# Kernel tuning notes

Measured on AMD Instinct MI355X. Metric: run time of the kernel, lower is better.

## Reference

```python
import jax, jax.numpy as jnp
import numpy as np

EPS = 1e-4
HEADS = 8
DIM_HEAD = 32
BALANCE = 0.3


def _normalize(x, dims):
    # torch normalize(): norm over `dims` in fp32; norm = eps + norm*sqrt(norm.numel()/x.numel())
    red = 1
    for d in dims:
        red *= x.shape[d]
    norm = jnp.sqrt(jnp.sum(jnp.square(x.astype(jnp.float32)), axis=dims, keepdims=True))
    norm = EPS + norm / np.sqrt(red)
    return x / norm.astype(x.dtype)


def _mpconv1x1(x, w, gain=1.0):
    # MPConv forward (eval mode): weight-normalize per output channel, scale, 1x1 conv
    w = w.astype(jnp.float32)
    w = _normalize(w, (1, 2, 3))
    fan_in = w.shape[1] * w.shape[2] * w.shape[3]
    w = (w * (gain / np.sqrt(fan_in))).astype(x.dtype)[:, :, 0, 0]  # [out, in]
    return jnp.einsum('oi,nihw->nohw', w, x)


def setup_inputs() -> dict:
    key = jax.random.key(0)
    k1, k2, k3 = jax.random.split(key, 3)
    x = jax.random.normal(k1, (2, 256, 48, 48), dtype=jnp.float32)
    w_qkv = jax.random.normal(k2, (768, 256, 1, 1), dtype=jnp.float32)
    w_out = jax.random.normal(k3, (256, 256, 1, 1), dtype=jnp.float32)
    return {"x": x, "w_qkv": w_qkv, "w_out": w_out}


def reference(x, w_qkv, w_out):
    n, c, h, w_sp = x.shape
    seq = h * w_sp
    y = _mpconv1x1(x, w_qkv)                          # [n, 3c, h, w]
    y = y.reshape(n, HEADS, DIM_HEAD, 3, seq)         # channel split: head x dim_head x 3
    y = _normalize(y, (2,))                           # L2-normalize over dim_head axis
    q = y[:, :, :, 0, :]
    k = y[:, :, :, 1, :]
    v = y[:, :, :, 2, :]
    # scores [n, h, q, k] with k scaled by 1/sqrt(dim_head)
    att = jax.nn.softmax(jnp.einsum('nhcq,nhck->nhqk', q, k) / np.sqrt(DIM_HEAD), axis=3)
    y = jnp.einsum('nhqk,nhck->nhcq', att, v)         # [n, heads, dim_head, seq]
    y = _mpconv1x1(y.reshape(n, c, h, w_sp), w_out)
    t = BALANCE
    # mp_sum: lerp then magnitude-preserving rescale
    return (x + t * (y - x)) / np.sqrt((1 - t) ** 2 + t ** 2)
```

## Files before the change

### kernel.cpp

```cpp
#include <hip/hip_runtime.h>
#include <math.h>

#define EPSN 1e-4f
#define SEQ 2304

using bf16x8 = __attribute__((ext_vector_type(8))) short;
using f32x4  = __attribute__((ext_vector_type(4))) float;

__device__ inline unsigned short f2bf(float x) {
    union { float f; unsigned u; } c; c.f = x;
    unsigned u = c.u;
    u += 0x7fffu + ((u >> 16) & 1u);
    return (unsigned short)(u >> 16);
}

__device__ inline unsigned cvt_pk_bf16(float lo, float hi) {
    unsigned r;
    asm("v_cvt_pk_bf16_f32 %0, %1, %2" : "=v"(r) : "v"(lo), "v"(hi));
    return r;
}
__device__ inline void permlane32_swap(unsigned &a, unsigned &b) {
    asm("v_permlane32_swap_b32 %0, %1" : "+v"(a), "+v"(b));
}
__device__ inline void permlane16_swap(unsigned &a, unsigned &b) {
    asm("v_permlane16_swap_b32 %0, %1" : "+v"(a), "+v"(b));
}

__global__ __launch_bounds__(256) void prep_w_kernel(const float* __restrict__ w_qkv,
                                                     const float* __restrict__ w_out,
                                                     unsigned short* __restrict__ wqb,
                                                     unsigned short* __restrict__ wob) {
    int wave = threadIdx.x >> 6, lane = threadIdx.x & 63;
    int row = blockIdx.x * 4 + wave;
    const float* src;
    unsigned short* dst;
    if (row < 768) { src = w_qkv + (size_t)row * 256; dst = wqb + (size_t)row * 256; }
    else           { src = w_out + (size_t)(row - 768) * 256; dst = wob + (size_t)(row - 768) * 256; }
    float4 v = *(const float4*)&src[lane * 4];
    float ss = v.x * v.x + v.y * v.y + v.z * v.z + v.w * v.w;
    for (int off = 32; off > 0; off >>= 1) ss += __shfl_xor(ss, off, 64);
    float sc = 1.0f / (sqrtf(ss) + 16.0f * EPSN);
    unsigned p0 = (unsigned)f2bf(v.x * sc) | ((unsigned)f2bf(v.y * sc) << 16);
    unsigned p1 = (unsigned)f2bf(v.z * sc) | ((unsigned)f2bf(v.w * sc) << 16);
    *(uint2*)&dst[lane * 4] = make_uint2(p0, p1);
}

__global__ __launch_bounds__(256) void qkv_fused_kernel(const float* __restrict__ x,
                                                        const unsigned short* __restrict__ wqb,
                                                        unsigned short* __restrict__ qn,
                                                        unsigned short* __restrict__ kn,
                                                        unsigned short* __restrict__ vn) {
    __shared__ __align__(16) unsigned short Xs[32][264];
    __shared__ float Cs[96][33];
    __shared__ __align__(16) unsigned short Vls[32][40];
    int bid = blockIdx.x;
    int xcd = bid & 7, j = bid >> 3;
    int h = j & 7;
    int tile = xcd * 18 + (j >> 3);
    int st2 = tile % 72, n = tile / 72;
    int tid = threadIdx.x;
    int wave = tid >> 6, lane = tid & 63;
    int ln = lane & 15, quad = lane >> 4;
    int sgrp = wave & 1, mgrp = wave >> 1;
    int s0 = st2 * 32;

    {
        int ci = tid >> 3, sv = (tid & 7) * 4;
#pragma unroll
        for (int p = 0; p < 8; ++p) {
            int c = p * 32 + ci;
            float4 v = *(const float4*)&x[(size_t)(n * 256 + c) * SEQ + s0 + sv];
            Xs[sv + 0][c] = f2bf(v.x);
            Xs[sv + 1][c] = f2bf(v.y);
            Xs[sv + 2][c] = f2bf(v.z);
            Xs[sv + 3][c] = f2bf(v.w);
        }
    }
    __syncthreads();

    const unsigned short* Abase = wqb + (size_t)(h * 96 + mgrp * 48 + ln) * 256 + quad * 8;
    f32x4 acc[3];
#pragma unroll
    for (int m = 0; m < 3; ++m) acc[m] = (f32x4){0.f, 0.f, 0.f, 0.f};
#pragma unroll
    for (int kc = 0; kc < 8; ++kc) {
        bf16x8 b = *(const bf16x8*)&Xs[sgrp * 16 + ln][kc * 32 + quad * 8];
#pragma unroll
        for (int m = 0; m < 3; ++m) {
            bf16x8 a = *(const bf16x8*)(Abase + (size_t)(m * 16) * 256 + kc * 32);
            acc[m] = __builtin_amdgcn_mfma_f32_16x16x32_bf16(a, b, acc[m], 0, 0, 0);
        }
    }
#pragma unroll
    for (int m = 0; m < 3; ++m)
#pragma unroll
        for (int r = 0; r < 4; ++r)
            Cs[mgrp * 48 + m * 16 + quad * 4 + r][sgrp * 16 + ln] = acc[m][r];
    __syncthreads();
    int nh = n * 8 + h;
    if (tid < 96) {
        int sl = tid & 31, wh = tid >> 5;
        int s = st2 * 32 + sl;
        float v[32];
        float ss = 0.f;
#pragma unroll
        for (int d = 0; d < 32; ++d) { v[d] = Cs[3 * d + wh][sl]; ss += v[d] * v[d]; }
        float inv = 1.0f / (EPSN + sqrtf(ss * (1.0f / 32.0f)));
        if (wh == 0) inv *= 0.17677669529663687f * 1.4426950408889634f;
        if (wh == 2) {
#pragma unroll
            for (int d = 0; d < 32; ++d) Vls[d][sl] = f2bf(v[d] * inv);
        } else {
            unsigned short* dst = (wh == 1 ? kn : qn) + (size_t)nh * 73728 + (size_t)s * 32;
            unsigned wbuf[16];
#pragma unroll
            for (int j2 = 0; j2 < 16; ++j2)
                wbuf[j2] = (unsigned)f2bf(v[2 * j2] * inv) | ((unsigned)f2bf(v[2 * j2 + 1] * inv) << 16);
#pragma unroll
            for (int j2 = 0; j2 < 4; ++j2) {
                uint4 t4 = make_uint4(wbuf[4 * j2], wbuf[4 * j2 + 1], wbuf[4 * j2 + 2], wbuf[4 * j2 + 3]);
                *(uint4*)(dst + j2 * 8) = t4;
            }
        }
    }
    __syncthreads();
    {
        int d = tid >> 3, sj = (tid & 7) * 4;
        uint2 t2 = *(const uint2*)&Vls[d][sj];
        *(uint2*)&vn[(size_t)nh * 73728 + (size_t)d * SEQ + st2 * 32 + sj] = t2;
    }
}

__global__ __launch_bounds__(256) void attn_mfma_kernel(const unsigned short* __restrict__ qn,
                                                        const unsigned short* __restrict__ kn,
                                                        const unsigned short* __restrict__ vn,
                                                        float* __restrict__ Opart,
                                                        float* __restrict__ Lpart) {
    int tid = threadIdx.x;
    int wq = tid >> 6, lane = tid & 63;
    int ln = lane & 15, quad = lane >> 4;
    int bid = blockIdx.x;
    int xcd = bid & 7, bi = bid >> 3;
    int nh = xcd * 2 + (bi >= 144);
    int bi2 = (bi >= 144) ? bi - 144 : bi;
    int qt = bi2 % 36, kz = bi2 / 36;
    const unsigned short* Qg = qn + (size_t)nh * 73728;
    const unsigned short* Kg = kn + (size_t)nh * 73728;
    const unsigned short* Vg = vn + (size_t)nh * 73728;

    bf16x8 qf = *(const bf16x8*)(Qg + (size_t)(qt * 64 + wq * 16 + ln) * 32 + quad * 8);
    bf16x8 ones;
#pragma unroll
    for (int i = 0; i < 8; ++i) ones[i] = (short)0x3F80;

    f32x4 o0 = {0.f, 0.f, 0.f, 0.f};
    f32x4 o1 = {0.f, 0.f, 0.f, 0.f};
    f32x4 lac = {0.f, 0.f, 0.f, 0.f};

    const int NT = 9;
    int s0 = kz * NT * 64;

    const unsigned short* Kb = Kg + (size_t)(s0 + ln) * 32 + quad * 8;
    const unsigned short* Vb = Vg + (size_t)ln * SEQ + s0 + quad * 8;

    for (int i = 0; i < NT; ++i) {
        const f32x4 zero = {0.f, 0.f, 0.f, 0.f};
        unsigned w[4][2];
#pragma unroll
        for (int c = 0; c < 4; ++c) {
            bf16x8 kf = *(const bf16x8*)(Kb + (size_t)(i * 64 + c * 16) * 32);
            f32x4 sc = __builtin_amdgcn_mfma_f32_16x16x32_bf16(kf, qf, zero, 0, 0, 0);
            w[c][0] = cvt_pk_bf16(exp2f(sc[0]), exp2f(sc[1]));
            w[c][1] = cvt_pk_bf16(exp2f(sc[2]), exp2f(sc[3]));
        }
#pragma unroll
        for (int kc = 0; kc < 2; ++kc) {
            unsigned a0 = w[2 * kc][0], b0 = w[2 * kc + 1][0];
            permlane32_swap(a0, b0);
            permlane16_swap(a0, b0);
            unsigned a1 = w[2 * kc][1], b1 = w[2 * kc + 1][1];
            permlane32_swap(a1, b1);
            permlane16_swap(a1, b1);
            union { unsigned u[4]; bf16x8 v8; } pk;
            pk.u[0] = a0; pk.u[1] = a1; pk.u[2] = b0; pk.u[3] = b1;
            bf16x8 v0 = *(const bf16x8*)(Vb + i * 64 + kc * 32);
            bf16x8 v1 = *(const bf16x8*)(Vb + (size_t)16 * SEQ + i * 64 + kc * 32);
            lac = __builtin_amdgcn_mfma_f32_16x16x32_bf16(pk.v8, ones, lac, 0, 0, 0);
            o0  = __builtin_amdgcn_mfma_f32_16x16x32_bf16(pk.v8, v0, o0, 0, 0, 0);
            o1  = __builtin_amdgcn_mfma_f32_16x16x32_bf16(pk.v8, v1, o1, 0, 0, 0);
        }
    }

    float* Ob = Opart + ((size_t)(kz * 16 + nh) * 36 + qt) * 2048;
    float* Lb = Lpart + ((size_t)(kz * 16 + nh) * 36 + qt) * 64;
#pragma unroll
    for (int r = 0; r < 4; ++r) {
        int ql = wq * 16 + quad * 4 + r;
        Ob[ql * 32 + ln]      = o0[r];
        Ob[ql * 32 + 16 + ln] = o1[r];
        if (ln == 0) Lb[ql] = lac[r];
    }
}

__global__ __launch_bounds__(256) void out_gemm_kernel(const float* __restrict__ Opart,
                                                       const float* __restrict__ Lpart,
                                                       const unsigned short* __restrict__ wob,
                                                       const float* __restrict__ x,
                                                       float* __restrict__ out) {
    __shared__ float Linv[8][16];
    __shared__ __align__(16) unsigned short Ys[16][264];
    int bid = blockIdx.x;
    int xcd = bid & 7, j = bid >> 3;
    int mt = j & 3;
    int u = j >> 2;
    int n = u & 1;
    int st = xcd * 18 + (u >> 1);
    int qt = st >> 2;
    int qo = (st & 3) * 16;
    int tid = threadIdx.x;

    if (tid < 128) {
        int h = tid >> 4, qi = tid & 15;
        size_t base = ((size_t)((n * 8 + h) * 36) + qt) * 64 + qo + qi;
        const size_t kzs = (size_t)16 * 36 * 64;
        float l = Lpart[base] + Lpart[base + kzs] + Lpart[base + 2 * kzs] + Lpart[base + 3 * kzs];
        Linv[h][qi] = 1.0f / l;
    }
    __syncthreads();
    {
        int qi = tid >> 4, dp = tid & 15, d0 = dp * 2;
        const size_t kzs = (size_t)16 * 36 * 2048;
#pragma unroll
        for (int h = 0; h < 8; ++h) {
            size_t ob = ((size_t)((n * 8 + h) * 36) + qt) * 2048 + (size_t)(qo + qi) * 32 + d0;
            float2 a = *(const float2*)&Opart[ob];
            float2 b = *(const float2*)&Opart[ob + kzs];
            float2 e = *(const float2*)&Opart[ob + 2 * kzs];
            float2 f = *(const float2*)&Opart[ob + 3 * kzs];
            float li = Linv[h][qi];
            float r0 = ((a.x + b.x) + (e.x + f.x)) * li;
            float r1 = ((a.y + b.y) + (e.y + f.y)) * li;
            *(unsigned*)&Ys[qi][h * 32 + d0] = cvt_pk_bf16(r0, r1);
        }
    }
    __syncthreads();

    int wave = tid >> 6, lane = tid & 63;
    int ln = lane & 15, quad = lane >> 4;
    int m0 = mt * 64 + wave * 16;
    const unsigned short* Abase = wob + (size_t)(m0 + ln) * 256 + quad * 8;
    f32x4 acc = (f32x4){0.f, 0.f, 0.f, 0.f};
#pragma unroll
    for (int kc = 0; kc < 8; ++kc) {
        bf16x8 a = *(const bf16x8*)(Abase + kc * 32);
        bf16x8 b = *(const bf16x8*)&Ys[ln][kc * 32 + quad * 8];
        acc = __builtin_amdgcn_mfma_f32_16x16x32_bf16(a, b, acc, 0, 0, 0);
    }
    const float c0f = 0.7f * 1.3130643285972254f;
    const float c1f = 0.3f * 1.3130643285972254f;
#pragma unroll
    for (int r = 0; r < 4; ++r) {
        int o = m0 + quad * 4 + r;
        int s = st * 16 + ln;
        size_t idx = (size_t)(n * 256 + o) * SEQ + s;
        out[idx] = c0f * x[idx] + c1f * acc[r];
    }
}

extern "C" void kernel_launch(void* const* d_in, const int* in_sizes, int n_in,
                              void* d_out, int out_size, void* d_ws, size_t ws_size,
                              hipStream_t stream) {
    (void)in_sizes; (void)n_in; (void)out_size; (void)ws_size;
    const float* x     = (const float*)d_in[0];
    const float* w_qkv = (const float*)d_in[1];
    const float* w_out = (const float*)d_in[2];
    float* out = (float*)d_out;
    float* ws  = (float*)d_ws;
    unsigned short* wqb = (unsigned short*)(ws);
    unsigned short* wob = (unsigned short*)(ws + 98304);
    unsigned short* qn  = (unsigned short*)(ws + 131072);
    unsigned short* kn  = (unsigned short*)(ws + 720896);
    unsigned short* vn  = (unsigned short*)(ws + 1310720);
    float* Opart = ws + 1900544;
    float* Lpart = ws + 6619136;

    hipLaunchKernelGGL(prep_w_kernel, dim3(256), dim3(256), 0, stream,
                       w_qkv, w_out, wqb, wob);
    hipLaunchKernelGGL(qkv_fused_kernel, dim3(1152), dim3(256), 0, stream,
                       x, wqb, qn, kn, vn);
    hipLaunchKernelGGL(attn_mfma_kernel, dim3(2304), dim3(256), 0, stream,
                       qn, kn, vn, Opart, Lpart);
    hipLaunchKernelGGL(out_gemm_kernel, dim3(1152), dim3(256), 0, stream,
                       Opart, Lpart, wob, x, out);
}
```

Baseline: 151.4 us.

## Stage K/V tiles in double-buffered LDS shared by two query tiles per block

The attention kernel now uses 512-thread blocks covering two 64-row query tiles, with half the blocks. Each K/V 64-key tile is loaded cooperatively from global memory once into LDS in an MFMA-friendly layout, then read by all eight waves. Register prefetch of the next tile is overlapped with compute through double buffering. This halves global K/V traffic and drops the strided per-lane V loads, at the cost of two barriers per tile and fewer blocks.

```diff
diff --git a/kernel.cpp b/kernel.cpp
--- a/kernel.cpp
+++ b/kernel.cpp
@@ -131,24 +131,28 @@
     }
 }
 
-__global__ __launch_bounds__(256) void attn_mfma_kernel(const unsigned short* __restrict__ qn,
+__global__ __launch_bounds__(512) void attn_mfma_kernel(const unsigned short* __restrict__ qn,
                                                         const unsigned short* __restrict__ kn,
                                                         const unsigned short* __restrict__ vn,
                                                         float* __restrict__ Opart,
                                                         float* __restrict__ Lpart) {
+    __shared__ __align__(16) unsigned char Ksm[2][4096];
+    __shared__ __align__(16) unsigned char Vsm[2][4096];
     int tid = threadIdx.x;
-    int wq = tid >> 6, lane = tid & 63;
+    int wave = tid >> 6, lane = tid & 63;
     int ln = lane & 15, quad = lane >> 4;
+    int wq = wave & 3;
     int bid = blockIdx.x;
     int xcd = bid & 7, bi = bid >> 3;
-    int nh = xcd * 2 + (bi >= 144);
-    int bi2 = (bi >= 144) ? bi - 144 : bi;
-    int qt = bi2 % 36, kz = bi2 / 36;
+    int nh = xcd * 2 + (bi >= 72);
+    int bi2 = (bi >= 72) ? bi - 72 : bi;
+    int qt = bi2 % 18, kz = bi2 / 18;
+    int qt64 = qt * 2 + (wave >> 2);
     const unsigned short* Qg = qn + (size_t)nh * 73728;
     const unsigned short* Kg = kn + (size_t)nh * 73728;
     const unsigned short* Vg = vn + (size_t)nh * 73728;
 
-    bf16x8 qf = *(const bf16x8*)(Qg + (size_t)(qt * 64 + wq * 16 + ln) * 32 + quad * 8);
+    bf16x8 qf = *(const bf16x8*)(Qg + (size_t)(qt64 * 64 + wq * 16 + ln) * 32 + quad * 8);
     bf16x8 ones;
 #pragma unroll
     for (int i = 0; i < 8; ++i) ones[i] = (short)0x3F80;
@@ -160,15 +164,29 @@
     const int NT = 9;
     int s0 = kz * NT * 64;
 
-    const unsigned short* Kb = Kg + (size_t)(s0 + ln) * 32 + quad * 8;
-    const unsigned short* Vb = Vg + (size_t)ln * SEQ + s0 + quad * 8;
-
-    for (int i = 0; i < NT; ++i) {
+    int ts = tid & 255;
+    bool isK = (tid < 256);
+    int kr = ts >> 2, kg = ts & 3;
+    int koff = ((kr >> 4) << 10) | (((kg << 4) | (kr & 15)) << 4);
+    int vd = ts >> 3, vg = ts & 7;
+    int voff = (((vg >> 2) * 2 + (vd >> 4)) << 10) | ((((vg & 3) << 4) | (vd & 15)) << 4);
+    int woff = isK ? koff : voff;
+    int lb = lane << 4;
+
+    auto gload = [&](int sn) -> uint4 {
+        return isK ? *(const uint4*)(Kg + (size_t)sn * 32 + ts * 8)
+                   : *(const uint4*)(Vg + (size_t)(ts >> 3) * SEQ + sn + (ts & 7) * 8);
+    };
+    auto swrite = [&](int buf, uint4 v) {
+        *(uint4*)((isK ? Ksm[buf] : Vsm[buf]) + woff) = v;
+    };
+
+    auto compute_tile = [&](int bsel) {
         const f32x4 zero = {0.f, 0.f, 0.f, 0.f};
         unsigned w[4][2];
 #pragma unroll
         for (int c = 0; c < 4; ++c) {
-            bf16x8 kf = *(const bf16x8*)(Kb + (size_t)(i * 64 + c * 16) * 32);
+            bf16x8 kf = *(const bf16x8*)(Ksm[bsel] + c * 1024 + lb);
             f32x4 sc = __builtin_amdgcn_mfma_f32_16x16x32_bf16(kf, qf, zero, 0, 0, 0);
             w[c][0] = cvt_pk_bf16(exp2f(sc[0]), exp2f(sc[1]));
             w[c][1] = cvt_pk_bf16(exp2f(sc[2]), exp2f(sc[3]));
@@ -183,16 +201,31 @@
             permlane16_swap(a1, b1);
             union { unsigned u[4]; bf16x8 v8; } pk;
             pk.u[0] = a0; pk.u[1] = a1; pk.u[2] = b0; pk.u[3] = b1;
-            bf16x8 v0 = *(const bf16x8*)(Vb + i * 64 + kc * 32);
-            bf16x8 v1 = *(const bf16x8*)(Vb + (size_t)16 * SEQ + i * 64 + kc * 32);
+            bf16x8 v0 = *(const bf16x8*)(Vsm[bsel] + (kc * 2 + 0) * 1024 + lb);
+            bf16x8 v1 = *(const bf16x8*)(Vsm[bsel] + (kc * 2 + 1) * 1024 + lb);
             lac = __builtin_amdgcn_mfma_f32_16x16x32_bf16(pk.v8, ones, lac, 0, 0, 0);
             o0  = __builtin_amdgcn_mfma_f32_16x16x32_bf16(pk.v8, v0, o0, 0, 0, 0);
             o1  = __builtin_amdgcn_mfma_f32_16x16x32_bf16(pk.v8, v1, o1, 0, 0, 0);
         }
-    }
-
-    float* Ob = Opart + ((size_t)(kz * 16 + nh) * 36 + qt) * 2048;
-    float* Lb = Lpart + ((size_t)(kz * 16 + nh) * 36 + qt) * 64;
+    };
+
+    uint4 rA = gload(s0);
+    swrite(0, rA);
+    uint4 rB = gload(s0 + 64);
+
+    for (int i = 0; i < NT; i += 2) {
+        if (i + 2 < NT) rA = gload(s0 + (i + 2) * 64);
+        __syncthreads();
+        compute_tile(0);
+        if (i + 1 < NT) swrite(1, rB);
+        if (i + 3 < NT) rB = gload(s0 + (i + 3) * 64);
+        __syncthreads();
+        if (i + 1 < NT) compute_tile(1);
+        if (i + 2 < NT) swrite(0, rA);
+    }
+
+    float* Ob = Opart + ((size_t)(kz * 16 + nh) * 36 + qt64) * 2048;
+    float* Lb = Lpart + ((size_t)(kz * 16 + nh) * 36 + qt64) * 64;
 #pragma unroll
     for (int r = 0; r < 4; ++r) {
         int ql = wq * 16 + quad * 4 + r;
@@ -288,7 +321,7 @@
                        w_qkv, w_out, wqb, wob);
     hipLaunchKernelGGL(qkv_fused_kernel, dim3(1152), dim3(256), 0, stream,
                        x, wqb, qn, kn, vn);
-    hipLaunchKernelGGL(attn_mfma_kernel, dim3(2304), dim3(256), 0, stream,
+    hipLaunchKernelGGL(attn_mfma_kernel, dim3(1152), dim3(512), 0, stream,
                        qn, kn, vn, Opart, Lpart);
     hipLaunchKernelGGL(out_gemm_kernel, dim3(1152), dim3(256), 0, stream,
                        Opart, Lpart, wob, x, out);
```

Result: faster. 123.9 us (-18.2%).
